# Kernel tuning notes

Hardware: AMD Instinct MI355X
Metric: run time of the kernel (lower is better)

Reference implementation:

```python
import jax, jax.numpy as jnp
import numpy as np

NQ = 4          # n_qubits
NL = 2          # n_layers
DIM = 2 ** NQ   # statevector dimension (16)
PI = np.float32(np.pi)

# H^{otimes NQ} (real, symmetric)
_H2 = np.array([[1.0, 1.0], [1.0, -1.0]], dtype=np.float32) / np.sqrt(2.0)
_M = _H2
for _ in range(NQ - 1):
    _M = np.kron(_M, _H2)
H_ALL = jnp.asarray(_M.astype(np.complex64))  # [DIM, DIM]

# z_i = +1/-1 eigenvalues per computational basis state; wire 0 is MSB (PennyLane)
_b = ((np.arange(DIM)[:, None] >> (NQ - 1 - np.arange(NQ))[None, :]) & 1)
Z = jnp.asarray((1.0 - 2.0 * _b).astype(np.float32))      # [DIM, NQ]
ZZ = Z[:, :-1] * Z[:, 1:]                                  # [DIM, NQ-1]


def _encode(angles):
    """Apply the ZZ feature map to |0...0>. angles: [..., NQ] -> state [..., DIM] complex64.

    Per layer: all Hadamards, then diagonal phase exp(-i/2 (sum th_i z_i + sum th_i th_{i+1} z_i z_{i+1}))
    (RZ and CNOT-RZ-CNOT = ZZ phase are diagonal; gates on distinct wires commute).
    """
    arg = (jnp.einsum('...q,dq->...d', angles, Z)
           + jnp.einsum('...p,dp->...d', angles[..., :-1] * angles[..., 1:], ZZ))
    diag = jnp.exp(arg * (-0.5j)).astype(jnp.complex64)     # [..., DIM]
    state = jnp.zeros(angles.shape[:-1] + (DIM,), jnp.complex64).at[..., 0].set(1.0)
    for _ in range(NL):
        state = state @ H_ALL      # H_ALL symmetric -> s @ H == H @ s
        state = state * diag
    return state


def setup_inputs() -> dict:
    key = jax.random.key(0)
    ks = jax.random.split(key, 7)
    B, L, S, H, D = 8, 1024, 1024, 8, 64
    return {
        'queries': jax.random.normal(ks[0], (B, L, H, D), jnp.float32),
        'keys':    jax.random.normal(ks[1], (B, S, H, D), jnp.float32),
        'values':  jax.random.normal(ks[2], (B, S, H, D), jnp.float32),
        'wq': jax.random.normal(ks[3], (NQ, D), jnp.float32) * 0.1,
        'bq': jax.random.normal(ks[4], (NQ,), jnp.float32) * 0.1,
        'wk': jax.random.normal(ks[5], (NQ, D), jnp.float32) * 0.1,
        'bk': jax.random.normal(ks[6], (NQ,), jnp.float32) * 0.1,
    }


def reference(queries, keys, values, wq, bq, wk, bk):
    # queries: [B,L,H,D], keys/values: [B,S,H,D]
    q_angles = jnp.tanh(queries @ wq.T + bq) * PI          # [B,L,H,NQ]
    k_angles = jnp.tanh(keys @ wk.T + bk) * PI             # [B,S,H,NQ]
    sq = _encode(q_angles.transpose(0, 2, 1, 3))           # [B,H,L,DIM] complex
    sk = _encode(k_angles.transpose(0, 2, 1, 3))           # [B,H,S,DIM] complex
    fid = jnp.einsum('bhld,bhsd->bhls', sq, jnp.conj(sk))  # overlap <phi_k|phi_q>
    attn_scores = (fid.real ** 2 + fid.imag ** 2).astype(queries.dtype)  # |.|^2 = probs[0]
    attn_weights = attn_scores / (attn_scores.sum(axis=-1, keepdims=True) + 1e-6)
    v = values.transpose(0, 2, 1, 3)                       # [B,H,S,D]
    context = jnp.einsum('bhls,bhsd->bhld', attn_weights, v).transpose(0, 2, 1, 3)
    return context, attn_weights
```

## Files before the change

### kernel.cpp

```cpp
#include <hip/hip_runtime.h>
#include <math.h>

#define PI_F 3.14159265358979323846f

constexpr int Bq = 8, Lq = 1024, Sq = 1024, Hq = 8, Dq = 64;

typedef short short8 __attribute__((ext_vector_type(8)));
typedef float f4v __attribute__((ext_vector_type(4)));
typedef unsigned short ushort_t;

static __device__ __forceinline__ ushort_t f2bf(float x) {
  union { float f; unsigned u; } v; v.f = x;
  unsigned r = v.u + 0x7fffu + ((v.u >> 16) & 1u);
  return (ushort_t)(r >> 16);
}
static __device__ __forceinline__ float bf2f(ushort_t b) {
  union { unsigned u; float f; } v; v.u = ((unsigned)b) << 16;
  return v.f;
}
static __device__ __forceinline__ f4v mfma16(short8 a, short8 b, f4v c) {
  return __builtin_amdgcn_mfma_f32_16x16x32_bf16(a, b, c, 0, 0, 0);
}
static __device__ __forceinline__ short8 primef(short8 q) {
  short8 r;
#pragma unroll
  for (int i = 0; i < 4; ++i) {
    r[2 * i]     = q[2 * i + 1];
    r[2 * i + 1] = (short)(((ushort_t)q[2 * i]) ^ 0x8000u);
  }
  return r;
}

static __device__ __forceinline__ void state_vec(
    const float* __restrict__ x, const float (*lw)[64], const float* lb,
    int n, float st[32])
{
  const float4* xp = (const float4*)(x + (size_t)n * 64);
  float a0 = lb[0], a1 = lb[1], a2 = lb[2], a3 = lb[3];
#pragma unroll
  for (int i = 0; i < 16; ++i) {
    float4 v = xp[i];
    a0 += v.x * lw[0][4*i] + v.y * lw[0][4*i+1] + v.z * lw[0][4*i+2] + v.w * lw[0][4*i+3];
    a1 += v.x * lw[1][4*i] + v.y * lw[1][4*i+1] + v.z * lw[1][4*i+2] + v.w * lw[1][4*i+3];
    a2 += v.x * lw[2][4*i] + v.y * lw[2][4*i+1] + v.z * lw[2][4*i+2] + v.w * lw[2][4*i+3];
    a3 += v.x * lw[3][4*i] + v.y * lw[3][4*i+1] + v.z * lw[3][4*i+2] + v.w * lw[3][4*i+3];
  }
  a0 = tanhf(a0) * PI_F; a1 = tanhf(a1) * PI_F;
  a2 = tanhf(a2) * PI_F; a3 = tanhf(a3) * PI_F;
  float p01 = a0 * a1, p12 = a1 * a2, p23 = a2 * a3;

  float dr[16], di[16];
#pragma unroll
  for (int d = 0; d < 16; ++d) {
    float s0 = (d & 8) ? -1.f : 1.f;
    float s1 = (d & 4) ? -1.f : 1.f;
    float s2 = (d & 2) ? -1.f : 1.f;
    float s3 = (d & 1) ? -1.f : 1.f;
    float arg = a0*s0 + a1*s1 + a2*s2 + a3*s3
              + p01*s0*s1 + p12*s1*s2 + p23*s2*s3;
    float sn, cs;
    sincosf(0.5f * arg, &sn, &cs);
    dr[d] = cs; di[d] = -sn;
  }
  float hr[16], hi[16];
#pragma unroll
  for (int i = 0; i < 16; ++i) { hr[i] = dr[i]; hi[i] = di[i]; }
#pragma unroll
  for (int stp = 1; stp < 16; stp <<= 1) {
#pragma unroll
    for (int i = 0; i < 16; ++i) {
      if (!(i & stp)) {
        float xr = hr[i], yr = hr[i + stp];
        hr[i] = xr + yr; hr[i + stp] = xr - yr;
        float xi = hi[i], yi = hi[i + stp];
        hi[i] = xi + yi; hi[i + stp] = xi - yi;
      }
    }
  }
#pragma unroll
  for (int d = 0; d < 16; ++d) {
    st[2*d]   = (dr[d] * hr[d] - di[d] * hi[d]) * 0.0625f;
    st[2*d+1] = (dr[d] * hi[d] + di[d] * hr[d]) * 0.0625f;
  }
}

__global__ __launch_bounds__(256) void k_prep(
    const float* __restrict__ qin, const float* __restrict__ kin,
    const float* __restrict__ vin,
    const float* __restrict__ wq, const float* __restrict__ bq,
    const float* __restrict__ wk, const float* __restrict__ bk,
    ushort_t* __restrict__ QH, ushort_t* __restrict__ QL,
    ushort_t* __restrict__ KFH, ushort_t* __restrict__ KFL,
    ushort_t* __restrict__ VFH)
{
  __shared__ float smem[64 * 68];
  int blk = blockIdx.x;
  int t = threadIdx.x;

  if (blk < 512) {
    const bool isQ = (blk < 256);
    const float* x    = isQ ? qin : kin;
    const float* w    = isQ ? wq : wk;
    const float* bias = isQ ? bq : bk;
    float (*lw)[64] = (float(*)[64])smem;
    float* lb = smem + 256;
    lw[t >> 6][t & 63] = w[t];
    if (t < 4) lb[t] = bias[t];
    __syncthreads();

    int n = (blk & 255) * 256 + t;
    float st[32];
    state_vec(x, lw, lb, n, st);
    int b = n >> 13, l = (n >> 3) & 1023, h = n & 7;
    int bh = b * 8 + h;

    unsigned hh[16], ll[16];
#pragma unroll
    for (int i = 0; i < 16; ++i) {
      ushort_t h0 = f2bf(st[2*i]), h1 = f2bf(st[2*i+1]);
      ushort_t e0 = f2bf(st[2*i] - bf2f(h0)), e1 = f2bf(st[2*i+1] - bf2f(h1));
      hh[i] = (unsigned)h0 | ((unsigned)h1 << 16);
      ll[i] = (unsigned)e0 | ((unsigned)e1 << 16);
    }
    if (isQ) {
      size_t rb = ((size_t)bh * Lq + l) * 32;
      uint4* ph = (uint4*)(QH + rb);
      uint4* pl = (uint4*)(QL + rb);
#pragma unroll
      for (int i = 0; i < 4; ++i) {
        ph[i] = make_uint4(hh[4*i], hh[4*i+1], hh[4*i+2], hh[4*i+3]);
        pl[i] = make_uint4(ll[4*i], ll[4*i+1], ll[4*i+2], ll[4*i+3]);
      }
    } else {
      int sf = l >> 4, lh = l & 15;
      size_t fb = (size_t)(bh * 64 + sf) * 512;
#pragma unroll
      for (int g = 0; g < 4; ++g) {
        size_t o = fb + (size_t)((g << 4) + lh) * 8;
        *(uint4*)(KFH + o) = make_uint4(hh[4*g], hh[4*g+1], hh[4*g+2], hh[4*g+3]);
        *(uint4*)(KFL + o) = make_uint4(ll[4*g], ll[4*g+1], ll[4*g+2], ll[4*g+3]);
      }
    }
  } else {
    int blk2 = blk - 512;
    int bh = blk2 >> 4, c = blk2 & 15;
    int b = bh >> 3, h = bh & 7;
    int s0 = c << 6;
    int sl = t >> 2, dq = (t & 3) << 4;
    const float4* src =
        (const float4*)(vin + (((size_t)b * Sq + s0 + sl) * Hq + h) * 64 + dq);
#pragma unroll
    for (int i = 0; i < 4; ++i)
      *(float4*)&smem[sl * 68 + dq + 4 * i] = src[i];
    __syncthreads();
#pragma unroll
    for (int sidx = 0; sidx < 2; ++sidx) {
      int slot = sidx * 256 + t;
      int ks = slot >> 8, f2 = (slot >> 6) & 3, lane = slot & 63;
      int lh = lane & 15, g = lane >> 4;
      int d = f2 * 16 + lh;
      unsigned w4[4];
#pragma unroll
      for (int e2 = 0; e2 < 4; ++e2) {
        int sl0 = ks * 32 + g * 8 + 2 * e2;
        w4[e2] = (unsigned)f2bf(smem[sl0 * 68 + d])
               | ((unsigned)f2bf(smem[(sl0 + 1) * 68 + d]) << 16);
      }
      size_t off = ((((size_t)(bh * 16 + c) * 2 + ks) * 4 + f2) * 64 + lane) * 8;
      *(uint4*)(VFH + off) = make_uint4(w4[0], w4[1], w4[2], w4[3]);
    }
  }
}

__global__ __launch_bounds__(256, 4) void k_fidpv4(
    const ushort_t* __restrict__ QH, const ushort_t* __restrict__ QL,
    const ushort_t* __restrict__ KFH, const ushort_t* __restrict__ KFL,
    const ushort_t* __restrict__ VFH, float* __restrict__ attn,
    float* __restrict__ ctx)
{
  __shared__ float Wtr[4][16 * 68];

  int bid = blockIdx.x;
  int xcd = bid & 7, idx = bid >> 3;
  int bh = (xcd << 3) | (idx >> 4);
  int l0 = (idx & 15) << 6;
  int t = threadIdx.x;
  int wv = t >> 6, lane = t & 63;
  int lh = lane & 15, g = lane >> 4, ko = g << 3;
  int rowbase = l0 + (wv << 4);

  size_t qoff = ((size_t)bh * Lq + rowbase + lh) * 32 + ko;
  short8 qh  = *(const short8*)(QH + qoff);
  short8 ql  = *(const short8*)(QL + qoff);
  short8 qph = primef(qh), qpl = primef(ql);

  const ushort_t* kfh = KFH + (size_t)bh * 32768 + (size_t)lane * 8;
  const ushort_t* kfl = KFL + (size_t)bh * 32768 + (size_t)lane * 8;
  const ushort_t* vfb = VFH + (size_t)bh * 65536 + (size_t)lane * 8;

  f4v zero = {0.f, 0.f, 0.f, 0.f};

  float rsum = 0.f;
#pragma unroll 8
  for (int sf = 0; sf < 64; ++sf) {
    short8 kh = *(const short8*)(kfh + sf * 512);
    f4v fr = mfma16(kh, qh, zero);
    f4v fi = mfma16(kh, qph, zero);
#pragma unroll
    for (int r = 0; r < 4; ++r) rsum += fr[r]*fr[r] + fi[r]*fi[r];
  }
  rsum += __shfl_xor(rsum, 16);
  rsum += __shfl_xor(rsum, 32);
  float rinv = 1.f / (rsum + 1e-6f);

  float* abase = attn + ((size_t)bh * Lq + rowbase) * Sq;
  float* wtr = &Wtr[wv][0];
  f4v acc[4] = {zero, zero, zero, zero};

  for (int c = 0; c < 16; ++c) {
    short8 kh[4], kl[4];
#pragma unroll
    for (int f = 0; f < 4; ++f) {
      kh[f] = *(const short8*)(kfh + (c * 4 + f) * 512);
      kl[f] = *(const short8*)(kfl + (c * 4 + f) * 512);
    }
    short8 vb[2][4];
#pragma unroll
    for (int ks = 0; ks < 2; ++ks)
#pragma unroll
      for (int f2 = 0; f2 < 4; ++f2)
        vb[ks][f2] = *(const short8*)(vfb + (size_t)(((c*2+ks)*4+f2)) * 512);

#pragma unroll
    for (int f = 0; f < 4; ++f) {
      f4v fr = mfma16(kh[f], qh, zero);
      fr = mfma16(kl[f], qh, fr);
      fr = mfma16(kh[f], ql, fr);
      f4v fi = mfma16(kh[f], qph, zero);
      fi = mfma16(kl[f], qph, fi);
      fi = mfma16(kh[f], qpl, fi);
      f4v wv4;
#pragma unroll
      for (int r = 0; r < 4; ++r)
        wv4[r] = (fr[r]*fr[r] + fi[r]*fi[r]) * rinv;
      *(f4v*)&wtr[lh * 68 + (f << 4) + (g << 2)] = wv4;
    }
#pragma unroll
    for (int j = 0; j < 4; ++j) {
      int rowp = (j << 2) + g;
      f4v vv = *(const f4v*)&wtr[rowp * 68 + (lh << 2)];
      __builtin_nontemporal_store(
          vv, (f4v*)(abase + (size_t)rowp * Sq + (c << 6) + (lh << 2)));
    }
#pragma unroll
    for (int ks = 0; ks < 2; ++ks) {
      f4v w0 = *(const f4v*)&wtr[lh * 68 + (ks << 5) + ko];
      f4v w1 = *(const f4v*)&wtr[lh * 68 + (ks << 5) + ko + 4];
      short8 wh;
#pragma unroll
      for (int e = 0; e < 4; ++e) wh[e] = (short)f2bf(w0[e]);
#pragma unroll
      for (int e = 0; e < 4; ++e) wh[4 + e] = (short)f2bf(w1[e]);
#pragma unroll
      for (int f2 = 0; f2 < 4; ++f2)
        acc[f2] = mfma16(wh, vb[ks][f2], acc[f2]);
    }
  }

  int b = bh >> 3, h = bh & 7;
#pragma unroll
  for (int f2 = 0; f2 < 4; ++f2) {
    int d = (f2 << 4) + lh;
#pragma unroll
    for (int r = 0; r < 4; ++r) {
      int l = rowbase + (g << 2) + r;
      ctx[(((size_t)b * Lq + l) * Hq + h) * 64 + d] = acc[f2][r];
    }
  }
}

extern "C" void kernel_launch(void* const* d_in, const int* in_sizes, int n_in,
                              void* d_out, int out_size, void* d_ws, size_t ws_size,
                              hipStream_t stream) {
  const float* q  = (const float*)d_in[0];
  const float* k  = (const float*)d_in[1];
  const float* v  = (const float*)d_in[2];
  const float* wq = (const float*)d_in[3];
  const float* bq = (const float*)d_in[4];
  const float* wk = (const float*)d_in[5];
  const float* bk = (const float*)d_in[6];

  float* out  = (float*)d_out;
  float* ctx  = out;
  float* attn = out + 4194304;

  char* wsb = (char*)d_ws;
  ushort_t* QH  = (ushort_t*)(wsb);
  ushort_t* QL  = (ushort_t*)(wsb + (size_t)4  * 1024 * 1024);
  ushort_t* KFH = (ushort_t*)(wsb + (size_t)8  * 1024 * 1024);
  ushort_t* KFL = (ushort_t*)(wsb + (size_t)12 * 1024 * 1024);
  ushort_t* VFH = (ushort_t*)(wsb + (size_t)16 * 1024 * 1024);

  hipLaunchKernelGGL(k_prep, dim3(1536), dim3(256), 0, stream,
                     q, k, v, wq, bq, wk, bk, QH, QL, KFH, KFL, VFH);
  hipLaunchKernelGGL(k_fidpv4, dim3(1024), dim3(256), 0, stream,
                     QH, QL, KFH, KFL, VFH, attn, ctx);
}
```

Before: 96.21 us.

## Stage K/V fragments through double-buffered LDS with async global-to-LDS loads

The fidelity/PV kernel now uses 512-thread blocks, each covering 128 query rows, so every K/V chunk is fetched once per block and shared by 8 waves instead of being loaded separately by each wave. Chunks are brought in with global_load_lds into a double-buffered LDS region, and the next chunk is prefetched while the current one is computed, guarded by explicit waitcnt and barriers. This cuts redundant global/L2 traffic for K and V and overlaps loads with MFMA work. In exchange it uses about 66 KB of LDS per block and adds a barrier every iteration, which can reduce occupancy and serialise the waves.

```diff
diff --git a/kernel.cpp b/kernel.cpp
--- a/kernel.cpp
+++ b/kernel.cpp
@@ -29,6 +29,11 @@
     r[2 * i + 1] = (short)(((ushort_t)q[2 * i]) ^ 0x8000u);
   }
   return r;
+}
+static __device__ __forceinline__ void gl_lds16(const void* g, void* l) {
+  __builtin_amdgcn_global_load_lds(
+      (const __attribute__((address_space(1))) unsigned int*)g,
+      (__attribute__((address_space(3))) unsigned int*)l, 16, 0, 0);
 }
 
 static __device__ __forceinline__ void state_vec(
@@ -172,18 +177,18 @@
   }
 }
 
-__global__ __launch_bounds__(256, 4) void k_fidpv4(
+__global__ __launch_bounds__(512, 4) void k_fidpv5(
     const ushort_t* __restrict__ QH, const ushort_t* __restrict__ QL,
     const ushort_t* __restrict__ KFH, const ushort_t* __restrict__ KFL,
     const ushort_t* __restrict__ VFH, float* __restrict__ attn,
     float* __restrict__ ctx)
 {
-  __shared__ float Wtr[4][16 * 68];
+  __shared__ char lds[67584];
 
   int bid = blockIdx.x;
   int xcd = bid & 7, idx = bid >> 3;
-  int bh = (xcd << 3) | (idx >> 4);
-  int l0 = (idx & 15) << 6;
+  int bh = (xcd << 3) | (idx >> 3);
+  int l0 = (idx & 7) << 7;
   int t = threadIdx.x;
   int wv = t >> 6, lane = t & 63;
   int lh = lane & 15, g = lane >> 4, ko = g << 3;
@@ -194,16 +199,33 @@
   short8 ql  = *(const short8*)(QL + qoff);
   short8 qph = primef(qh), qpl = primef(ql);
 
-  const ushort_t* kfh = KFH + (size_t)bh * 32768 + (size_t)lane * 8;
-  const ushort_t* kfl = KFL + (size_t)bh * 32768 + (size_t)lane * 8;
-  const ushort_t* vfb = VFH + (size_t)bh * 65536 + (size_t)lane * 8;
+  const ushort_t* gKH = KFH + (size_t)bh * 32768 + (size_t)lane * 8;
+  const ushort_t* gKL = KFL + (size_t)bh * 32768 + (size_t)lane * 8;
+  const ushort_t* gV  = VFH + (size_t)bh * 65536 + (size_t)lane * 8;
+
+  float* wtr = (float*)(lds + 32768) + wv * 1088;
 
   f4v zero = {0.f, 0.f, 0.f, 0.f};
+
+#define FP_STAGE(p, cc) do {                                        \
+    int fi0_ = wv << 1;                                             \
+    _Pragma("unroll")                                               \
+    for (int j_ = 0; j_ < 2; ++j_) {                                \
+      int fi_ = fi0_ + j_;                                          \
+      const ushort_t* g_;                                           \
+      if (fi_ < 4)      g_ = gKH + ((cc) * 4 + fi_) * 512;          \
+      else if (fi_ < 8) g_ = gKL + ((cc) * 4 + (fi_ - 4)) * 512;    \
+      else              g_ = gV  + ((cc) * 8 + (fi_ - 8)) * 512;    \
+      gl_lds16(g_, lds + (p) * 16384 + fi_ * 1024);                 \
+    }                                                               \
+  } while (0)
+
+  FP_STAGE(0, 0);
 
   float rsum = 0.f;
 #pragma unroll 8
   for (int sf = 0; sf < 64; ++sf) {
-    short8 kh = *(const short8*)(kfh + sf * 512);
+    short8 kh = *(const short8*)(gKH + sf * 512);
     f4v fr = mfma16(kh, qh, zero);
     f4v fi = mfma16(kh, qph, zero);
 #pragma unroll
@@ -214,22 +236,27 @@
   float rinv = 1.f / (rsum + 1e-6f);
 
   float* abase = attn + ((size_t)bh * Lq + rowbase) * Sq;
-  float* wtr = &Wtr[wv][0];
   f4v acc[4] = {zero, zero, zero, zero};
 
   for (int c = 0; c < 16; ++c) {
-    short8 kh[4], kl[4];
+    if (c == 0) asm volatile("s_waitcnt vmcnt(0)" ::: "memory");
+    else        asm volatile("s_waitcnt vmcnt(4)" ::: "memory");
+    __builtin_amdgcn_s_barrier();
+    __builtin_amdgcn_sched_barrier(0);
+    if (c < 15) FP_STAGE((c + 1) & 1, c + 1);
+
+    const char* base = lds + (c & 1) * 16384;
+    short8 kh[4], kl[4], vb[2][4];
 #pragma unroll
     for (int f = 0; f < 4; ++f) {
-      kh[f] = *(const short8*)(kfh + (c * 4 + f) * 512);
-      kl[f] = *(const short8*)(kfl + (c * 4 + f) * 512);
-    }
-    short8 vb[2][4];
+      kh[f] = *(const short8*)(base + f * 1024 + lane * 16);
+      kl[f] = *(const short8*)(base + 4096 + f * 1024 + lane * 16);
+    }
 #pragma unroll
     for (int ks = 0; ks < 2; ++ks)
 #pragma unroll
       for (int f2 = 0; f2 < 4; ++f2)
-        vb[ks][f2] = *(const short8*)(vfb + (size_t)(((c*2+ks)*4+f2)) * 512);
+        vb[ks][f2] = *(const short8*)(base + 8192 + (ks * 4 + f2) * 1024 + lane * 16);
 
 #pragma unroll
     for (int f = 0; f < 4; ++f) {
@@ -265,7 +292,9 @@
       for (int f2 = 0; f2 < 4; ++f2)
         acc[f2] = mfma16(wh, vb[ks][f2], acc[f2]);
     }
-  }
+    asm volatile("s_waitcnt lgkmcnt(0)" ::: "memory");
+  }
+#undef FP_STAGE
 
   int b = bh >> 3, h = bh & 7;
 #pragma unroll
@@ -303,6 +332,6 @@
 
   hipLaunchKernelGGL(k_prep, dim3(1536), dim3(256), 0, stream,
                      q, k, v, wq, bq, wk, bk, QH, QL, KFH, KFL, VFH);
-  hipLaunchKernelGGL(k_fidpv4, dim3(1024), dim3(256), 0, stream,
+  hipLaunchKernelGGL(k_fidpv5, dim3(512), dim3(512), 0, stream,
                      QH, QL, KFH, KFL, VFH, attn, ctx);
 }
```

Measured after the change: 104.4 us. +8.5%, slower.
